# Optimization experiments

Hardware: AMD Instinct MI355X
Metric: run time of the kernel (lower is better)

Reference implementation:

```python
import math
import jax, jax.numpy as jnp
import numpy as np

HEAD_DIM = 128
NUM_HEADS = 16
NUM_KV_HEADS = 4
CAUSAL = True


def rotate_half(x):
    x1 = x[..., : x.shape[-1] // 2]
    x2 = x[..., x.shape[-1] // 2 :]
    return jnp.concatenate([-x2, x1], axis=-1)


def setup_inputs() -> dict:
    key = jax.random.key(0)
    k1, k2, k3, k4, k5 = jax.random.split(key, 5)
    B, S, H = 2, 2048, 2048
    total_heads = NUM_HEADS + 2 * NUM_KV_HEADS  # 24
    hidden_states = jax.random.normal(k1, (B, S, H), dtype=jnp.float32)
    cos = jax.random.normal(k2, (S, HEAD_DIM), dtype=jnp.float32)
    sin = jax.random.normal(k3, (S, HEAD_DIM), dtype=jnp.float32)
    # eqx.nn.Linear weight layout: [out_features, in_features], y = W @ x
    w_qkv = jax.random.normal(k4, (total_heads * HEAD_DIM, H), dtype=jnp.float32) / math.sqrt(H)
    w_o = jax.random.normal(k5, (H, NUM_HEADS * HEAD_DIM), dtype=jnp.float32) / math.sqrt(NUM_HEADS * HEAD_DIM)
    return {"hidden_states": hidden_states, "cos": cos, "sin": sin, "w_qkv": w_qkv, "w_o": w_o}


def reference(hidden_states, cos, sin, w_qkv, w_o):
    B, S, _ = hidden_states.shape
    # fused QKV projection: [B,S,total_heads,head_dim]
    qkv = jnp.einsum("bsh,oh->bso", hidden_states, w_qkv).reshape(B, S, -1, HEAD_DIM)
    q = qkv[:, :, :NUM_HEADS]
    k = qkv[:, :, NUM_HEADS : NUM_HEADS + NUM_KV_HEADS]
    v = qkv[:, :, NUM_HEADS + NUM_KV_HEADS :]
    # RoPE: cos/sin [S,head_dim] -> broadcast [S,1,head_dim] over heads
    c = cos[..., None, :]
    s_ = sin[..., None, :]
    q = q * c + rotate_half(q) * s_
    k = k * c + rotate_half(k) * s_
    # GQA: repeat K/V across query-head groups
    rep = NUM_HEADS // NUM_KV_HEADS
    k = jnp.repeat(k, rep, axis=2)
    v = jnp.repeat(v, rep, axis=2)
    scale = 1.0 / math.sqrt(HEAD_DIM)
    scores = jnp.einsum("bshd,bthd->bhst", q, k) * scale  # [B,H,S,S]
    if CAUSAL:
        mask = jnp.tril(jnp.ones((S, S), dtype=bool))[None, None]
        scores = jnp.where(mask, scores, jnp.float32(-1e10))
    attn = jax.nn.softmax(scores, axis=-1)
    out = jnp.einsum("bhst,bthd->bshd", attn, v).reshape(B, S, -1)
    return jnp.einsum("bsd,od->bso", out, w_o)
```

## Files before the change

kernel.cpp:

```cpp
#include <hip/hip_runtime.h>
#include <hip/hip_bf16.h>
#include <stdint.h>

typedef __hip_bfloat16 bf16;
typedef __attribute__((ext_vector_type(8))) __bf16 bf16x8;
typedef __attribute__((ext_vector_type(4))) float f32x4;
typedef __attribute__((ext_vector_type(16))) float f32x16;
typedef __attribute__((ext_vector_type(4))) unsigned int u32x4;

#define QSCALE_LOG2E (0.08838834764831845f * 1.4426950408889634f)

__device__ __forceinline__ float fast_exp2(float x) {
#if __has_builtin(__builtin_amdgcn_exp2f)
  return __builtin_amdgcn_exp2f(x);
#else
  return exp2f(x);
#endif
}

__device__ __forceinline__ void gload_lds16(const void* g, void* l) {
  __builtin_amdgcn_global_load_lds(
      (__attribute__((address_space(1))) void*)(uintptr_t)g,
      (__attribute__((address_space(3))) void*)(uint32_t)(uintptr_t)l,
      16, 0, 0);
}

__global__ void cast3(const float* __restrict__ h, const float* __restrict__ wq,
                      const float* __restrict__ wo, bf16* __restrict__ oh,
                      bf16* __restrict__ owq, bf16* __restrict__ owo) {
  const int total = 4718592;
  const int stride = gridDim.x * blockDim.x;
  for (int c = blockIdx.x * blockDim.x + threadIdx.x; c < total; c += stride) {
    const float* src;
    bf16* dst;
    int i;
    if (c < 2097152) { src = h; dst = oh; i = c; }
    else if (c < 3670016) { src = wq; dst = owq; i = c - 2097152; }
    else { src = wo; dst = owo; i = c - 3670016; }
    float4 v = reinterpret_cast<const float4*>(src)[i];
    bf16 tmp[4];
    tmp[0] = __float2bfloat16(v.x);
    tmp[1] = __float2bfloat16(v.y);
    tmp[2] = __float2bfloat16(v.z);
    tmp[3] = __float2bfloat16(v.w);
    reinterpret_cast<uint2*>(dst)[i] = *reinterpret_cast<uint2*>(tmp);
  }
}

__device__ __forceinline__ void store_c(float v, bf16* p) { *p = __float2bfloat16(v); }
__device__ __forceinline__ void store_c(float v, float* p) { *p = v; }

__device__ __forceinline__ bf16x8 rd_swz(const bf16* base, int row, int ks, int hi) {
  const int byte = row * 128 + ((ks * 64 + hi * 16) ^ ((row & 7) << 4));
  return *reinterpret_cast<const bf16x8*>((const char*)base + byte);
}

__device__ __forceinline__ void stage_part(const bf16* __restrict__ g, int K,
                                           int kt, bf16* ldsBase, int part,
                                           int tid) {
  const int ga = part * 512 + tid;
  const int r = ga >> 3;
  const int gl = ga & 7;
  const int col = kt * 64 + ((gl ^ (r & 7)) << 3);
  gload_lds16(g + (size_t)r * K + col, (char*)ldsBase + ga * 16);
}

#define DS_A(QR)                                                              \
  _Pragma("unroll") for (int m = 0; m < 4; ++m)                               \
  _Pragma("unroll") for (int ks = 0; ks < 2; ++ks)                            \
      af[m][ks] = rd_swz(Acur, wm * 128 + (QR) * 64 + m * 16 + lr, ks, hi);

#define DS_B0()                                                               \
  _Pragma("unroll") for (int n = 0; n < NQ0; ++n)                             \
  _Pragma("unroll") for (int ks = 0; ks < 2; ++ks)                            \
      bf0[n][ks] = rd_swz(Bcur, wn * WN + n * 16 + lr, ks, hi);

#define DS_B1()                                                               \
  _Pragma("unroll") for (int n = 0; n < NQ1; ++n)                             \
  _Pragma("unroll") for (int ks = 0; ks < 2; ++ks)                            \
      bf1[n][ks] = rd_swz(Bcur, wn * WN + (NQ0 + n) * 16 + lr, ks, hi);

#define MFMA_Q0(QR)                                                           \
  __builtin_amdgcn_s_setprio(1);                                             \
  _Pragma("unroll") for (int ks = 0; ks < 2; ++ks)                            \
  _Pragma("unroll") for (int m = 0; m < 4; ++m)                               \
  _Pragma("unroll") for (int n = 0; n < NQ0; ++n)                             \
      acc[(QR) * 4 + m][n] = __builtin_amdgcn_mfma_f32_16x16x32_bf16(         \
          af[m][ks], bf0[n][ks], acc[(QR) * 4 + m][n], 0, 0, 0);              \
  __builtin_amdgcn_s_setprio(0);

#define MFMA_Q1(QR)                                                           \
  __builtin_amdgcn_s_setprio(1);                                             \
  _Pragma("unroll") for (int ks = 0; ks < 2; ++ks)                            \
  _Pragma("unroll") for (int m = 0; m < 4; ++m)                               \
  _Pragma("unroll") for (int n = 0; n < NQ1; ++n)                             \
      acc[(QR) * 4 + m][NQ0 + n] = __builtin_amdgcn_mfma_f32_16x16x32_bf16(   \
          af[m][ks], bf1[n][ks], acc[(QR) * 4 + m][NQ0 + n], 0, 0, 0);        \
  __builtin_amdgcn_s_setprio(0);

#define PHASE_SYNC_PRE()                                \
  __builtin_amdgcn_s_barrier();                         \
  asm volatile("s_waitcnt lgkmcnt(0)" ::: "memory");    \
  __builtin_amdgcn_sched_barrier(0);

#define PHASE_END() __builtin_amdgcn_s_barrier();

template <int BN, typename OutT>
__global__ __launch_bounds__(512, 2) void gemm256(const bf16* __restrict__ A,
                                                  const bf16* __restrict__ B,
                                                  OutT* __restrict__ C,
                                                  int M, int N, int K, int NBX) {
  constexpr int NFRAG = BN / 64;
  constexpr int NQ0 = (NFRAG + 1) / 2;
  constexpr int NQ1 = NFRAG - NQ0;
  constexpr int WN = BN / 4;
  constexpr int LB = BN / 64;
  constexpr int LB1 = (LB > 2) ? 2 : LB;
  constexpr int LB2 = LB - LB1;

  extern __shared__ bf16 sm[];
  bf16* Ab = sm;
  bf16* Bb = sm + 3 * 16384;

  const int tid = threadIdx.x;
  const int lane = tid & 63;
  const int w = tid >> 6;
  const int wm = w >> 2;
  const int wn = w & 3;
  const int lr = lane & 15;
  const int hi = lane >> 4;

  const int nwg = gridDim.x;
  const int cpx = nwg >> 3;
  const int bid = blockIdx.x;
  const int wg = (bid & 7) * cpx + (bid >> 3);
  const int bx = wg % NBX;
  const int by = wg / NBX;
  const int row0 = by * 256;
  const int col0 = bx * BN;

  const bf16* Ag = A + (size_t)row0 * K;
  const bf16* Bg = B + (size_t)col0 * K;

#pragma unroll
  for (int p = 0; p < 4; ++p) stage_part(Ag, K, 0, Ab, p, tid);
#pragma unroll
  for (int p = 0; p < 4; ++p) stage_part(Ag, K, 1, Ab + 16384, p, tid);
#pragma unroll
  for (int p = 0; p < LB; ++p) stage_part(Bg, K, 0, Bb, p, tid);
  asm volatile("s_waitcnt vmcnt(0)" ::: "memory");
  __builtin_amdgcn_s_barrier();

  f32x4 acc[8][NFRAG] = {};
  bf16x8 af[4][2], bf0[NQ0][2], bf1[NQ1 ? NQ1 : 1][2];

  const int ntile = K >> 6;
  for (int t = 0; t < ntile; ++t) {
    const bf16* Acur = Ab + (t % 3) * 16384;
    const bf16* Bcur = Bb + (t & 1) * (BN * 64);
    bf16* Bnext = Bb + ((t + 1) & 1) * (BN * 64);
    bf16* Anext2 = Ab + ((t + 2) % 3) * 16384;
    const bool sB = (t + 1 < ntile);
    const bool sA = (t + 2 < ntile);
    DS_A(0); DS_B0();
    if (sB) {
#pragma unroll
      for (int p = 0; p < LB1; ++p) stage_part(Bg, K, t + 1, Bnext, p, tid);
    }
    PHASE_SYNC_PRE(); MFMA_Q0(0); PHASE_END();
    DS_B1();
    if (sB && LB2 > 0) {
#pragma unroll
      for (int p = 0; p < LB2; ++p)
        stage_part(Bg, K, t + 1, Bnext, LB1 + p, tid);
    }
    PHASE_SYNC_PRE(); MFMA_Q1(0); PHASE_END();
    DS_A(1);
    if (sA) {
      stage_part(Ag, K, t + 2, Anext2, 0, tid);
      stage_part(Ag, K, t + 2, Anext2, 1, tid);
    }
    PHASE_SYNC_PRE(); MFMA_Q0(1); PHASE_END();
    if (sA) {
      stage_part(Ag, K, t + 2, Anext2, 2, tid);
      stage_part(Ag, K, t + 2, Anext2, 3, tid);
      asm volatile("s_waitcnt vmcnt(4)" ::: "memory");
    } else {
      asm volatile("s_waitcnt vmcnt(0)" ::: "memory");
    }
    PHASE_SYNC_PRE(); MFMA_Q1(1); PHASE_END();
  }

#pragma unroll
  for (int mi = 0; mi < 8; ++mi)
#pragma unroll
    for (int ni = 0; ni < NFRAG; ++ni)
#pragma unroll
      for (int j = 0; j < 4; ++j) {
        const int r = row0 + wm * 128 + mi * 16 + hi * 4 + j;
        const int cc = col0 + wn * WN + ni * 16 + lr;
        store_c(acc[mi][ni][j], &C[(size_t)r * N + cc]);
      }
}

__global__ void rope_scatter(const bf16* __restrict__ qkv,
                             const float* __restrict__ cs,
                             const float* __restrict__ sn,
                             bf16* __restrict__ Q, bf16* __restrict__ Kd) {
  const int tok = blockIdx.x;
  const int b = tok >> 11;
  const int s = tok & 2047;
  const bf16* row = qkv + (size_t)tok * 3072;
  for (int idx = threadIdx.x; idx < 1280; idx += blockDim.x) {
    const int head = idx >> 6;
    const int j = idx & 63;
    float x1 = __bfloat162float(row[head * 128 + j]);
    float x2 = __bfloat162float(row[head * 128 + j + 64]);
    const float c1 = cs[s * 128 + j];
    const float c2 = cs[s * 128 + j + 64];
    const float s1 = sn[s * 128 + j];
    const float s2 = sn[s * 128 + j + 64];
    float y1 = x1 * c1 - x2 * s1;
    float y2 = x2 * c2 + x1 * s2;
    bf16* dst;
    if (head < 16) {
      y1 *= QSCALE_LOG2E;
      y2 *= QSCALE_LOG2E;
      dst = Q + ((size_t)(b * 16 + head) * 2048 + s) * 128;
    } else {
      dst = Kd + ((size_t)(b * 4 + head - 16) * 2048 + s) * 128;
    }
    dst[j] = __float2bfloat16(y1);
    dst[j + 64] = __float2bfloat16(y2);
  }
}

__global__ __launch_bounds__(256) void vtrans(const bf16* __restrict__ qkv,
                                              bf16* __restrict__ Vt) {
  __shared__ bf16 tile[64 * 136];
  const int bid = blockIdx.x;
  const int stile = bid & 31;
  const int hv = (bid >> 5) & 3;
  const int b = bid >> 7;
  const int tid = threadIdx.x;
  const int tok0 = stile * 64;
  const bf16* src = qkv + (size_t)(b * 2048 + tok0) * 3072 + 2560 + hv * 128;
#pragma unroll
  for (int i = 0; i < 4; ++i) {
    const int c = tid + i * 256;
    const int r = c >> 4;
    const int off = (c & 15) * 8;
    uint4 d = *reinterpret_cast<const uint4*>(src + (size_t)r * 3072 + off);
    *reinterpret_cast<uint4*>(&tile[r * 136 + off]) = d;
  }
  __syncthreads();
  bf16* dst = Vt + ((size_t)(b * 4 + hv) * 128) * 2048 + tok0;
#pragma unroll
  for (int i = 0; i < 4; ++i) {
    const int o = tid + i * 256;
    const int d = o >> 3;
    const int s0 = (o & 7) * 8;
    bf16 vals[8];
#pragma unroll
    for (int j = 0; j < 8; ++j) vals[j] = tile[(s0 + j) * 136 + d];
    *reinterpret_cast<uint4*>(dst + (size_t)d * 2048 + s0) =
        *reinterpret_cast<const uint4*>(vals);
  }
}

__device__ __forceinline__ void stage_k(const bf16* __restrict__ Kb, int k0,
                                        bf16* dst, int w, int lane) {
#pragma unroll
  for (int i = 0; i < 4; ++i) {
    const int L16 = i * 256 + w * 64 + lane;
    const int row = L16 >> 4;
    const int colb = (L16 & 15) * 16;
    const int src = colb ^ ((row & 7) << 4);
    gload_lds16(Kb + (size_t)(k0 + row) * 128 + (src >> 1),
                (char*)dst + (i * 256 + w * 64) * 16);
  }
}

__device__ __forceinline__ void stage_v(const bf16* __restrict__ Vtb, int k0,
                                        bf16* dst, int w, int lane) {
#pragma unroll
  for (int i = 0; i < 4; ++i) {
    const int L16 = i * 256 + w * 64 + lane;
    const int row = L16 >> 3;
    const int colb = (L16 & 7) * 16;
    const int src = colb ^ ((row & 7) << 4);
    gload_lds16(Vtb + (size_t)row * 2048 + k0 + (src >> 1),
                (char*)dst + (i * 256 + w * 64) * 16);
  }
}

__device__ __forceinline__ bf16x8 lds_read_swz(const bf16* base, int row,
                                               int colElem, int rowBytes) {
  const int byte = row * rowBytes + (((colElem * 2) ^ ((row & 7) << 4)));
  return *reinterpret_cast<const bf16x8*>((const char*)base + byte);
}

__global__ __launch_bounds__(256, 2) void attn_fwd(const bf16* __restrict__ Qg,
                                                   const bf16* __restrict__ Kg,
                                                   const bf16* __restrict__ Vtg,
                                                   bf16* __restrict__ Og) {
  __shared__ bf16 Ks[2][64 * 128];
  __shared__ bf16 Vs[2][128 * 64];

  const int tid = threadIdx.x;
  const int lane = tid & 63;
  const int w = tid >> 6;
  const int bid = blockIdx.x;
  int qt, bh;
  if (bid < 256) { qt = bid & 15; bh = bid >> 4; }
  else           { qt = 15 - (bid & 15); bh = 16 + ((bid - 256) >> 4); }
  const int b = bh >> 4;
  const int h = bh & 15;
  const int kvh = h >> 2;
  const int q31 = lane & 31;
  const int hw = lane >> 5;

  const bf16* Qb = Qg + ((size_t)(b * 16 + h) * 2048) * 128;
  const bf16* Kb = Kg + ((size_t)(b * 4 + kvh) * 2048) * 128;
  const bf16* Vtb = Vtg + ((size_t)(b * 4 + kvh) * 128) * 2048;

  const int qw = qt * 128 + w * 32;

  bf16x8 qf[8];
#pragma unroll
  for (int db = 0; db < 8; ++db)
    qf[db] = *reinterpret_cast<const bf16x8*>(Qb + (size_t)(qw + q31) * 128 +
                                              db * 16 + hw * 8);

  f32x16 acc[4] = {};
  float mrow = -1e30f;
  float lsum = 0.f;

  const int nt = 2 * qt + 2;

  stage_k(Kb, 0, &Ks[0][0], w, lane);
  stage_v(Vtb, 0, &Vs[0][0], w, lane);

  for (int t = 0; t < nt; ++t) {
    const int cur = t & 1;
    if (t + 1 < nt) {
      stage_k(Kb, (t + 1) * 64, &Ks[cur ^ 1][0], w, lane);
      stage_v(Vtb, (t + 1) * 64, &Vs[cur ^ 1][0], w, lane);
      asm volatile("s_waitcnt vmcnt(8)" ::: "memory");
    } else {
      asm volatile("s_waitcnt vmcnt(0)" ::: "memory");
    }
    __builtin_amdgcn_s_barrier();
    __builtin_amdgcn_sched_barrier(0);

    const int k0 = t * 64;
    const bool active = (k0 <= qw + 31);
    if (active) {
      const bf16* Kt = &Ks[cur][0];
      const bf16* Vtl = &Vs[cur][0];

      f32x16 sacc[2] = {};
#pragma unroll
      for (int kb = 0; kb < 2; ++kb)
#pragma unroll
        for (int db = 0; db < 8; ++db) {
          bf16x8 kf = lds_read_swz(Kt, kb * 32 + q31, db * 16 + hw * 8, 256);
          sacc[kb] = __builtin_amdgcn_mfma_f32_32x32x16_bf16(kf, qf[db],
                                                             sacc[kb], 0, 0, 0);
        }

      float p[2][16];
#pragma unroll
      for (int kb = 0; kb < 2; ++kb)
#pragma unroll
        for (int r = 0; r < 16; ++r) p[kb][r] = sacc[kb][r];

      if (k0 + 63 > qw) {
        const int qg = qw + q31;
#pragma unroll
        for (int kb = 0; kb < 2; ++kb)
#pragma unroll
          for (int r = 0; r < 16; ++r) {
            const int k = k0 + kb * 32 + (r & 3) + 8 * (r >> 2) + 4 * hw;
            if (k > qg) p[kb][r] = -1e30f;
          }
      }

      float mt = p[0][0];
#pragma unroll
      for (int r = 1; r < 16; ++r) mt = fmaxf(mt, p[0][r]);
#pragma unroll
      for (int r = 0; r < 16; ++r) mt = fmaxf(mt, p[1][r]);
      mt = fmaxf(mt, __shfl_xor(mt, 32));

      if (__any(mt > mrow + 11.5f)) {
        const float mnew = fmaxf(mrow, mt);
        const float alpha = fast_exp2(mrow - mnew);
        mrow = mnew;
        lsum *= alpha;
        float areg[16];
#pragma unroll
        for (int r = 0; r < 16; ++r) {
          const int qloc = (r & 3) + 8 * (r >> 2) + 4 * hw;
          areg[r] = __shfl(alpha, qloc + (lane & 32));
        }
#pragma unroll
        for (int db = 0; db < 4; ++db)
#pragma unroll
          for (int r = 0; r < 16; ++r) acc[db][r] *= areg[r];
      }

      float rs = 0.f;
#pragma unroll
      for (int kb = 0; kb < 2; ++kb)
#pragma unroll
        for (int r = 0; r < 16; ++r) {
          const float pe = fast_exp2(p[kb][r] - mrow);
          p[kb][r] = pe;
          rs += pe;
        }
      rs += __shfl_xor(rs, 32);
      lsum += rs;

      unsigned int pk[2][8];
#pragma unroll
      for (int kb = 0; kb < 2; ++kb)
#pragma unroll
        for (int i = 0; i < 8; ++i)
          asm("v_cvt_pk_bf16_f32 %0, %1, %2"
              : "=v"(pk[kb][i])
              : "v"(p[kb][2 * i]), "v"(p[kb][2 * i + 1]));

#pragma unroll
      for (int kb16 = 0; kb16 < 4; ++kb16) {
        const int kb = kb16 >> 1;
        const int j0 = (kb16 & 1) * 4;
        unsigned int a0 = pk[kb][j0 + 0], b0 = pk[kb][j0 + 2];
        unsigned int a1 = pk[kb][j0 + 1], b1 = pk[kb][j0 + 3];
        asm volatile("v_permlane32_swap_b32 %0, %1" : "+v"(a0), "+v"(b0));
        asm volatile("v_permlane32_swap_b32 %0, %1" : "+v"(a1), "+v"(b1));
        u32x4 afu;
        afu.x = a0; afu.y = a1; afu.z = b0; afu.w = b1;
        bf16x8 pa;
        __builtin_memcpy(&pa, &afu, 16);
#pragma unroll
        for (int db = 0; db < 4; ++db) {
          bf16x8 vf = lds_read_swz(Vtl, db * 32 + q31, kb16 * 16 + hw * 8, 128);
          acc[db] = __builtin_amdgcn_mfma_f32_32x32x16_bf16(pa, vf,
                                                            acc[db], 0, 0, 0);
        }
      }
    }

    __builtin_amdgcn_sched_barrier(0);
    __builtin_amdgcn_s_barrier();
  }

  const float inv = 1.0f / lsum;
  float invq[16];
#pragma unroll
  for (int r = 0; r < 16; ++r) {
    const int qloc = (r & 3) + 8 * (r >> 2) + 4 * hw;
    invq[r] = __shfl(inv, qloc + (lane & 32));
  }
#pragma unroll
  for (int db = 0; db < 4; ++db)
#pragma unroll
    for (int r = 0; r < 16; ++r) {
      const int qg = qw + (r & 3) + 8 * (r >> 2) + 4 * hw;
      const int dg = db * 32 + q31;
      Og[((size_t)(b * 2048 + qg)) * 2048 + h * 128 + dg] =
          __float2bfloat16(acc[db][r] * invq[r]);
    }
}

extern "C" void kernel_launch(void* const* d_in, const int* in_sizes, int n_in,
                              void* d_out, int out_size, void* d_ws,
                              size_t ws_size, hipStream_t stream) {
  const float* hidden = (const float*)d_in[0];
  const float* cs = (const float*)d_in[1];
  const float* sn = (const float*)d_in[2];
  const float* wqkv = (const float*)d_in[3];
  const float* wo = (const float*)d_in[4];
  float* out = (float*)d_out;

  bf16* p = (bf16*)d_ws;
  bf16* hid_b = p;   p += 8388608;
  bf16* wqkv_b = p;  p += 6291456;
  bf16* wo_b = p;    p += 4194304;
  bf16* qkv = p;     p += 12582912;
  bf16* Qs = p;      p += 8388608;
  bf16* Ksc = p;     p += 2097152;
  bf16* Vt = p;      p += 2097152;

  (void)hipFuncSetAttribute((const void*)gemm256<192, bf16>,
                            hipFuncAttributeMaxDynamicSharedMemorySize, 147456);
  (void)hipFuncSetAttribute((const void*)gemm256<128, float>,
                            hipFuncAttributeMaxDynamicSharedMemorySize, 131072);

  cast3<<<2048, 256, 0, stream>>>(hidden, wqkv, wo, hid_b, wqkv_b, wo_b);

  gemm256<192, bf16><<<256, 512, 147456, stream>>>(hid_b, wqkv_b, qkv,
                                                   4096, 3072, 2048, 16);
  rope_scatter<<<4096, 256, 0, stream>>>(qkv, cs, sn, Qs, Ksc);
  vtrans<<<256, 256, 0, stream>>>(qkv, Vt);

  bf16* aout = hid_b;
  attn_fwd<<<512, 256, 0, stream>>>(Qs, Ksc, Vt, aout);

  gemm256<128, float><<<256, 512, 131072, stream>>>(aout, wo_b, out,
                                                    4096, 2048, 2048, 16);
}
```

Before: 178.4 us.

## Restructure GEMM phase schedule with triple-buffered B and fuse rope/vtrans launches

Rewrites the GEMM main loop into explicit phases. For BN=128, B gets a third LDS buffer and is prefetched two tiles ahead, and K-steps run in two MFMA phases instead of four, with all A stages issued together. For BN=192 the third column fragment is handled in its own phase. The separate rope_scatter and vtrans kernels are merged into one launch that branches on block index, removing one kernel launch. This costs more LDS for the output GEMM, which may limit occupancy.

```diff
diff --git a/kernel.cpp b/kernel.cpp
--- a/kernel.cpp
+++ b/kernel.cpp
@@ -65,39 +65,6 @@
   gload_lds16(g + (size_t)r * K + col, (char*)ldsBase + ga * 16);
 }
 
-#define DS_A(QR)                                                              \
-  _Pragma("unroll") for (int m = 0; m < 4; ++m)                               \
-  _Pragma("unroll") for (int ks = 0; ks < 2; ++ks)                            \
-      af[m][ks] = rd_swz(Acur, wm * 128 + (QR) * 64 + m * 16 + lr, ks, hi);
-
-#define DS_B0()                                                               \
-  _Pragma("unroll") for (int n = 0; n < NQ0; ++n)                             \
-  _Pragma("unroll") for (int ks = 0; ks < 2; ++ks)                            \
-      bf0[n][ks] = rd_swz(Bcur, wn * WN + n * 16 + lr, ks, hi);
-
-#define DS_B1()                                                               \
-  _Pragma("unroll") for (int n = 0; n < NQ1; ++n)                             \
-  _Pragma("unroll") for (int ks = 0; ks < 2; ++ks)                            \
-      bf1[n][ks] = rd_swz(Bcur, wn * WN + (NQ0 + n) * 16 + lr, ks, hi);
-
-#define MFMA_Q0(QR)                                                           \
-  __builtin_amdgcn_s_setprio(1);                                             \
-  _Pragma("unroll") for (int ks = 0; ks < 2; ++ks)                            \
-  _Pragma("unroll") for (int m = 0; m < 4; ++m)                               \
-  _Pragma("unroll") for (int n = 0; n < NQ0; ++n)                             \
-      acc[(QR) * 4 + m][n] = __builtin_amdgcn_mfma_f32_16x16x32_bf16(         \
-          af[m][ks], bf0[n][ks], acc[(QR) * 4 + m][n], 0, 0, 0);              \
-  __builtin_amdgcn_s_setprio(0);
-
-#define MFMA_Q1(QR)                                                           \
-  __builtin_amdgcn_s_setprio(1);                                             \
-  _Pragma("unroll") for (int ks = 0; ks < 2; ++ks)                            \
-  _Pragma("unroll") for (int m = 0; m < 4; ++m)                               \
-  _Pragma("unroll") for (int n = 0; n < NQ1; ++n)                             \
-      acc[(QR) * 4 + m][NQ0 + n] = __builtin_amdgcn_mfma_f32_16x16x32_bf16(   \
-          af[m][ks], bf1[n][ks], acc[(QR) * 4 + m][NQ0 + n], 0, 0, 0);        \
-  __builtin_amdgcn_s_setprio(0);
-
 #define PHASE_SYNC_PRE()                                \
   __builtin_amdgcn_s_barrier();                         \
   asm volatile("s_waitcnt lgkmcnt(0)" ::: "memory");    \
@@ -106,17 +73,15 @@
 #define PHASE_END() __builtin_amdgcn_s_barrier();
 
 template <int BN, typename OutT>
-__global__ __launch_bounds__(512, 2) void gemm256(const bf16* __restrict__ A,
+__global__ __launch_bounds__(512, 2) void gemm_dp(const bf16* __restrict__ A,
                                                   const bf16* __restrict__ B,
                                                   OutT* __restrict__ C,
                                                   int M, int N, int K, int NBX) {
   constexpr int NFRAG = BN / 64;
-  constexpr int NQ0 = (NFRAG + 1) / 2;
-  constexpr int NQ1 = NFRAG - NQ0;
   constexpr int WN = BN / 4;
   constexpr int LB = BN / 64;
-  constexpr int LB1 = (LB > 2) ? 2 : LB;
-  constexpr int LB2 = LB - LB1;
+  constexpr int NBB = (NFRAG == 2) ? 3 : 2;
+  constexpr int AB = (NFRAG == 2) ? 2 : 1;
 
   extern __shared__ bf16 sm[];
   bf16* Ab = sm;
@@ -148,47 +113,116 @@
   for (int p = 0; p < 4; ++p) stage_part(Ag, K, 1, Ab + 16384, p, tid);
 #pragma unroll
   for (int p = 0; p < LB; ++p) stage_part(Bg, K, 0, Bb, p, tid);
+  if constexpr (NFRAG == 2) {
+#pragma unroll
+    for (int p = 0; p < LB; ++p) stage_part(Bg, K, 1, Bb + BN * 64, p, tid);
+  }
   asm volatile("s_waitcnt vmcnt(0)" ::: "memory");
   __builtin_amdgcn_s_barrier();
 
   f32x4 acc[8][NFRAG] = {};
-  bf16x8 af[4][2], bf0[NQ0][2], bf1[NQ1 ? NQ1 : 1][2];
+  bf16x8 af[8][2], bfv[2][2], bf2[2];
 
   const int ntile = K >> 6;
   for (int t = 0; t < ntile; ++t) {
     const bf16* Acur = Ab + (t % 3) * 16384;
-    const bf16* Bcur = Bb + (t & 1) * (BN * 64);
-    bf16* Bnext = Bb + ((t + 1) & 1) * (BN * 64);
-    bf16* Anext2 = Ab + ((t + 2) % 3) * 16384;
-    const bool sB = (t + 1 < ntile);
+    const bf16* Bcur = Bb + (t % NBB) * (BN * 64);
+    bf16* Adst = Ab + ((t + 2) % 3) * 16384;
+    bf16* Bdst = Bb + ((t + AB) % NBB) * (BN * 64);
     const bool sA = (t + 2 < ntile);
-    DS_A(0); DS_B0();
+    const bool sB = (t + AB < ntile);
+
+#pragma unroll
+    for (int m = 0; m < 4; ++m)
+#pragma unroll
+      for (int ks = 0; ks < 2; ++ks)
+        af[m][ks] = rd_swz(Acur, wm * 128 + m * 16 + lr, ks, hi);
+#pragma unroll
+    for (int n = 0; n < 2; ++n)
+#pragma unroll
+      for (int ks = 0; ks < 2; ++ks)
+        bfv[n][ks] = rd_swz(Bcur, wn * WN + n * 16 + lr, ks, hi);
     if (sB) {
 #pragma unroll
-      for (int p = 0; p < LB1; ++p) stage_part(Bg, K, t + 1, Bnext, p, tid);
-    }
-    PHASE_SYNC_PRE(); MFMA_Q0(0); PHASE_END();
-    DS_B1();
-    if (sB && LB2 > 0) {
-#pragma unroll
-      for (int p = 0; p < LB2; ++p)
-        stage_part(Bg, K, t + 1, Bnext, LB1 + p, tid);
-    }
-    PHASE_SYNC_PRE(); MFMA_Q1(0); PHASE_END();
-    DS_A(1);
-    if (sA) {
-      stage_part(Ag, K, t + 2, Anext2, 0, tid);
-      stage_part(Ag, K, t + 2, Anext2, 1, tid);
-    }
-    PHASE_SYNC_PRE(); MFMA_Q0(1); PHASE_END();
-    if (sA) {
-      stage_part(Ag, K, t + 2, Anext2, 2, tid);
-      stage_part(Ag, K, t + 2, Anext2, 3, tid);
-      asm volatile("s_waitcnt vmcnt(4)" ::: "memory");
+      for (int p = 0; p < LB; ++p) stage_part(Bg, K, t + AB, Bdst, p, tid);
+    }
+    PHASE_SYNC_PRE();
+    __builtin_amdgcn_s_setprio(1);
+#pragma unroll
+    for (int ks = 0; ks < 2; ++ks)
+#pragma unroll
+      for (int m = 0; m < 4; ++m)
+#pragma unroll
+        for (int n = 0; n < 2; ++n)
+          acc[m][n] = __builtin_amdgcn_mfma_f32_16x16x32_bf16(
+              af[m][ks], bfv[n][ks], acc[m][n], 0, 0, 0);
+    __builtin_amdgcn_s_setprio(0);
+    PHASE_END();
+
+#pragma unroll
+    for (int m = 0; m < 4; ++m)
+#pragma unroll
+      for (int ks = 0; ks < 2; ++ks)
+        af[4 + m][ks] = rd_swz(Acur, wm * 128 + 64 + m * 16 + lr, ks, hi);
+    if constexpr (NFRAG == 2) {
+      if (sA) {
+#pragma unroll
+        for (int p = 0; p < 4; ++p) stage_part(Ag, K, t + 2, Adst, p, tid);
+        asm volatile("s_waitcnt vmcnt(6)" ::: "memory");
+      } else {
+        asm volatile("s_waitcnt vmcnt(0)" ::: "memory");
+      }
+      PHASE_SYNC_PRE();
+      __builtin_amdgcn_s_setprio(1);
+#pragma unroll
+      for (int ks = 0; ks < 2; ++ks)
+#pragma unroll
+        for (int m = 0; m < 4; ++m)
+#pragma unroll
+          for (int n = 0; n < 2; ++n)
+            acc[4 + m][n] = __builtin_amdgcn_mfma_f32_16x16x32_bf16(
+                af[4 + m][ks], bfv[n][ks], acc[4 + m][n], 0, 0, 0);
+      __builtin_amdgcn_s_setprio(0);
+      PHASE_END();
     } else {
-      asm volatile("s_waitcnt vmcnt(0)" ::: "memory");
-    }
-    PHASE_SYNC_PRE(); MFMA_Q1(1); PHASE_END();
+      if (sA) {
+        stage_part(Ag, K, t + 2, Adst, 0, tid);
+        stage_part(Ag, K, t + 2, Adst, 1, tid);
+      }
+      PHASE_SYNC_PRE();
+      __builtin_amdgcn_s_setprio(1);
+#pragma unroll
+      for (int ks = 0; ks < 2; ++ks)
+#pragma unroll
+        for (int m = 0; m < 4; ++m)
+#pragma unroll
+          for (int n = 0; n < 2; ++n)
+            acc[4 + m][n] = __builtin_amdgcn_mfma_f32_16x16x32_bf16(
+                af[4 + m][ks], bfv[n][ks], acc[4 + m][n], 0, 0, 0);
+      __builtin_amdgcn_s_setprio(0);
+      PHASE_END();
+
+#pragma unroll
+      for (int ks = 0; ks < 2; ++ks)
+        bf2[ks] = rd_swz(Bcur, wn * WN + 32 + lr, ks, hi);
+      if (sA) {
+        stage_part(Ag, K, t + 2, Adst, 2, tid);
+        stage_part(Ag, K, t + 2, Adst, 3, tid);
+        asm volatile("s_waitcnt vmcnt(4)" ::: "memory");
+      } else {
+        asm volatile("s_waitcnt vmcnt(0)" ::: "memory");
+      }
+      PHASE_SYNC_PRE();
+      __builtin_amdgcn_s_setprio(1);
+#pragma unroll
+      for (int ks = 0; ks < 2; ++ks)
+#pragma unroll
+        for (int m = 0; m < 8; ++m)
+          acc[m][NFRAG - 1] = __builtin_amdgcn_mfma_f32_16x16x32_bf16(
+              af[m][ks], bf2[ks], acc[m][NFRAG - 1], 0, 0, 0);
+      __builtin_amdgcn_s_setprio(0);
+      PHASE_END();
+    }
   }
 
 #pragma unroll
@@ -203,68 +237,70 @@
       }
 }
 
-__global__ void rope_scatter(const bf16* __restrict__ qkv,
-                             const float* __restrict__ cs,
-                             const float* __restrict__ sn,
-                             bf16* __restrict__ Q, bf16* __restrict__ Kd) {
-  const int tok = blockIdx.x;
-  const int b = tok >> 11;
-  const int s = tok & 2047;
-  const bf16* row = qkv + (size_t)tok * 3072;
-  for (int idx = threadIdx.x; idx < 1280; idx += blockDim.x) {
-    const int head = idx >> 6;
-    const int j = idx & 63;
-    float x1 = __bfloat162float(row[head * 128 + j]);
-    float x2 = __bfloat162float(row[head * 128 + j + 64]);
-    const float c1 = cs[s * 128 + j];
-    const float c2 = cs[s * 128 + j + 64];
-    const float s1 = sn[s * 128 + j];
-    const float s2 = sn[s * 128 + j + 64];
-    float y1 = x1 * c1 - x2 * s1;
-    float y2 = x2 * c2 + x1 * s2;
-    bf16* dst;
-    if (head < 16) {
-      y1 *= QSCALE_LOG2E;
-      y2 *= QSCALE_LOG2E;
-      dst = Q + ((size_t)(b * 16 + head) * 2048 + s) * 128;
-    } else {
-      dst = Kd + ((size_t)(b * 4 + head - 16) * 2048 + s) * 128;
-    }
-    dst[j] = __float2bfloat16(y1);
-    dst[j + 64] = __float2bfloat16(y2);
-  }
-}
-
-__global__ __launch_bounds__(256) void vtrans(const bf16* __restrict__ qkv,
-                                              bf16* __restrict__ Vt) {
+__global__ __launch_bounds__(256) void rope_vtrans(const bf16* __restrict__ qkv,
+                                                   const float* __restrict__ cs,
+                                                   const float* __restrict__ sn,
+                                                   bf16* __restrict__ Q,
+                                                   bf16* __restrict__ Kd,
+                                                   bf16* __restrict__ Vt) {
   __shared__ bf16 tile[64 * 136];
   const int bid = blockIdx.x;
-  const int stile = bid & 31;
-  const int hv = (bid >> 5) & 3;
-  const int b = bid >> 7;
-  const int tid = threadIdx.x;
-  const int tok0 = stile * 64;
-  const bf16* src = qkv + (size_t)(b * 2048 + tok0) * 3072 + 2560 + hv * 128;
-#pragma unroll
-  for (int i = 0; i < 4; ++i) {
-    const int c = tid + i * 256;
-    const int r = c >> 4;
-    const int off = (c & 15) * 8;
-    uint4 d = *reinterpret_cast<const uint4*>(src + (size_t)r * 3072 + off);
-    *reinterpret_cast<uint4*>(&tile[r * 136 + off]) = d;
-  }
-  __syncthreads();
-  bf16* dst = Vt + ((size_t)(b * 4 + hv) * 128) * 2048 + tok0;
-#pragma unroll
-  for (int i = 0; i < 4; ++i) {
-    const int o = tid + i * 256;
-    const int d = o >> 3;
-    const int s0 = (o & 7) * 8;
-    bf16 vals[8];
-#pragma unroll
-    for (int j = 0; j < 8; ++j) vals[j] = tile[(s0 + j) * 136 + d];
-    *reinterpret_cast<uint4*>(dst + (size_t)d * 2048 + s0) =
-        *reinterpret_cast<const uint4*>(vals);
+  if (bid < 4096) {
+    const int tok = bid;
+    const int b = tok >> 11;
+    const int s = tok & 2047;
+    const bf16* row = qkv + (size_t)tok * 3072;
+    for (int idx = threadIdx.x; idx < 1280; idx += blockDim.x) {
+      const int head = idx >> 6;
+      const int j = idx & 63;
+      float x1 = __bfloat162float(row[head * 128 + j]);
+      float x2 = __bfloat162float(row[head * 128 + j + 64]);
+      const float c1 = cs[s * 128 + j];
+      const float c2 = cs[s * 128 + j + 64];
+      const float s1 = sn[s * 128 + j];
+      const float s2 = sn[s * 128 + j + 64];
+      float y1 = x1 * c1 - x2 * s1;
+      float y2 = x2 * c2 + x1 * s2;
+      bf16* dst;
+      if (head < 16) {
+        y1 *= QSCALE_LOG2E;
+        y2 *= QSCALE_LOG2E;
+        dst = Q + ((size_t)(b * 16 + head) * 2048 + s) * 128;
+      } else {
+        dst = Kd + ((size_t)(b * 4 + head - 16) * 2048 + s) * 128;
+      }
+      dst[j] = __float2bfloat16(y1);
+      dst[j + 64] = __float2bfloat16(y2);
+    }
+  } else {
+    const int vb = bid - 4096;
+    const int stile = vb & 31;
+    const int hv = (vb >> 5) & 3;
+    const int b = vb >> 7;
+    const int tid = threadIdx.x;
+    const int tok0 = stile * 64;
+    const bf16* src = qkv + (size_t)(b * 2048 + tok0) * 3072 + 2560 + hv * 128;
+#pragma unroll
+    for (int i = 0; i < 4; ++i) {
+      const int c = tid + i * 256;
+      const int r = c >> 4;
+      const int off = (c & 15) * 8;
+      uint4 d = *reinterpret_cast<const uint4*>(src + (size_t)r * 3072 + off);
+      *reinterpret_cast<uint4*>(&tile[r * 136 + off]) = d;
+    }
+    __syncthreads();
+    bf16* dst = Vt + ((size_t)(b * 4 + hv) * 128) * 2048 + tok0;
+#pragma unroll
+    for (int i = 0; i < 4; ++i) {
+      const int o = tid + i * 256;
+      const int d = o >> 3;
+      const int s0 = (o & 7) * 8;
+      bf16 vals[8];
+#pragma unroll
+      for (int j = 0; j < 8; ++j) vals[j] = tile[(s0 + j) * 136 + d];
+      *reinterpret_cast<uint4*>(dst + (size_t)d * 2048 + s0) =
+          *reinterpret_cast<const uint4*>(vals);
+    }
   }
 }
 
@@ -493,21 +529,20 @@
   bf16* Ksc = p;     p += 2097152;
   bf16* Vt = p;      p += 2097152;
 
-  (void)hipFuncSetAttribute((const void*)gemm256<192, bf16>,
+  (void)hipFuncSetAttribute((const void*)gemm_dp<192, bf16>,
                             hipFuncAttributeMaxDynamicSharedMemorySize, 147456);
-  (void)hipFuncSetAttribute((const void*)gemm256<128, float>,
-                            hipFuncAttributeMaxDynamicSharedMemorySize, 131072);
+  (void)hipFuncSetAttribute((const void*)gemm_dp<128, float>,
+                            hipFuncAttributeMaxDynamicSharedMemorySize, 147456);
 
   cast3<<<2048, 256, 0, stream>>>(hidden, wqkv, wo, hid_b, wqkv_b, wo_b);
 
-  gemm256<192, bf16><<<256, 512, 147456, stream>>>(hid_b, wqkv_b, qkv,
+  gemm_dp<192, bf16><<<256, 512, 147456, stream>>>(hid_b, wqkv_b, qkv,
                                                    4096, 3072, 2048, 16);
-  rope_scatter<<<4096, 256, 0, stream>>>(qkv, cs, sn, Qs, Ksc);
-  vtrans<<<256, 256, 0, stream>>>(qkv, Vt);
+  rope_vtrans<<<4352, 256, 0, stream>>>(qkv, cs, sn, Qs, Ksc, Vt);
 
   bf16* aout = hid_b;
   attn_fwd<<<512, 256, 0, stream>>>(Qs, Ksc, Vt, aout);
 
-  gemm256<128, float><<<256, 512, 131072, stream>>>(aout, wo_b, out,
+  gemm_dp<128, float><<<256, 512, 147456, stream>>>(aout, wo_b, out,
                                                     4096, 2048, 2048, 16);
 }
```

Result: no change. 177.0 us (-0.8%).
